# Kernel tuning notes

Hardware: AMD Instinct MI355X
Metric: run time of the kernel (lower is better)

Reference implementation:

```python
import jax, jax.numpy as jnp
import numpy as np

B, S, D = 2, 1024, 2048
H, KV, HD = 16, 4, 128
GROUPS = H // KV
THETA = 10000.0


def act_quant(xr, xi):
    # per-token 8-bit absmax quantization over last dim, joint scale for re/im, STE
    amax = jnp.maximum(jnp.max(jnp.abs(xr), -1, keepdims=True),
                       jnp.max(jnp.abs(xi), -1, keepdims=True))
    s = 127.0 / jnp.maximum(amax, 1e-5)
    qr = jnp.clip(jnp.round(xr * s), -128, 127) / s
    qi = jnp.clip(jnp.round(xi * s), -128, 127) / s
    return xr + jax.lax.stop_gradient(qr - xr), xi + jax.lax.stop_gradient(qi - xi)


def weight_quant(wr, wi):
    # Fairy+-i direction quantization: each weight -> scale * d, d in {+1,-1,+i,-i}; STE
    mag = jnp.mean(jnp.sqrt(wr * wr + wi * wi))
    use_re = jnp.abs(wr) >= jnp.abs(wi)
    qr = jnp.where(use_re, jnp.sign(wr) * mag, 0.0)
    qi = jnp.where(use_re, 0.0, jnp.sign(wi) * mag)
    return wr + jax.lax.stop_gradient(qr - wr), wi + jax.lax.stop_gradient(qi - wi)


def complex_linear(xr, xi, wr, wi):
    xr, xi = act_quant(xr, xi)
    wr, wi = weight_quant(wr, wi)
    o_re = xr @ wr - xi @ wi
    o_im = xr @ wi + xi @ wr
    return o_re, o_im


def rotate_half(x):
    h = x.shape[-1] // 2
    return jnp.concatenate([-x[..., h:], x[..., :h]], axis=-1)


def rope_tables():
    inv_freq = 1.0 / (THETA ** (jnp.arange(0, HD, 2, dtype=jnp.float32) / HD))
    pos = jnp.arange(S, dtype=jnp.float32)
    freqs = pos[:, None] * inv_freq[None, :]          # [S, HD/2]
    emb = jnp.concatenate([freqs, freqs], axis=-1)    # [S, HD]
    return jnp.cos(emb)[None, None], jnp.sin(emb)[None, None]  # [1,1,S,HD]


def _heads(x, n):
    # [B,S,n*HD] -> [B,n,S,HD]
    return x.reshape(B, S, n, HD).transpose(0, 2, 1, 3)


def _attn(hidden_real, hidden_imag, wq_re, wq_im, wk_re, wk_im,
          wv_re, wv_im, wo_re, wo_im):
    q_re, q_im = complex_linear(hidden_real, hidden_imag, wq_re, wq_im)
    k_re, k_im = complex_linear(hidden_real, hidden_imag, wk_re, wk_im)
    v_re, v_im = complex_linear(hidden_real, hidden_imag, wv_re, wv_im)

    q_re, q_im = _heads(q_re, H), _heads(q_im, H)      # [B,H,S,HD]
    k_re, k_im = _heads(k_re, KV), _heads(k_im, KV)    # [B,KV,S,HD]
    v_re, v_im = _heads(v_re, KV), _heads(v_im, KV)

    cos, sin = rope_tables()
    # RoPE applied only to real components of q and k
    q_re = q_re * cos + rotate_half(q_re) * sin
    k_re = k_re * cos + rotate_half(k_re) * sin

    # GQA repeat
    k_re = jnp.repeat(k_re, GROUPS, axis=1)
    k_im = jnp.repeat(k_im, GROUPS, axis=1)
    v_re = jnp.repeat(v_re, GROUPS, axis=1)
    v_im = jnp.repeat(v_im, GROUPS, axis=1)

    # real scores = Re(q . conj(k)) = q_re.k_re + q_im.k_im
    scores = (jnp.einsum('bhqd,bhkd->bhqk', q_re, k_re) +
              jnp.einsum('bhqd,bhkd->bhqk', q_im, k_im)) / jnp.sqrt(jnp.float32(HD))
    causal = jnp.tril(jnp.ones((S, S), dtype=bool))
    scores = jnp.where(causal[None, None], scores, jnp.finfo(scores.dtype).min)
    attn = jax.nn.softmax(scores, axis=-1)

    o_re = jnp.einsum('bhqk,bhkd->bhqd', attn, v_re)
    o_im = jnp.einsum('bhqk,bhkd->bhqd', attn, v_im)
    o_re = o_re.transpose(0, 2, 1, 3).reshape(B, S, H * HD)
    o_im = o_im.transpose(0, 2, 1, 3).reshape(B, S, H * HD)

    out_re, out_im = complex_linear(o_re, o_im, wo_re, wo_im)
    return jnp.stack([out_re, out_im])  # [2,B,S,D]


def setup_inputs() -> dict:
    key = jax.random.key(0)
    ks = jax.random.split(key, 12)
    w = lambda k, shp: jax.random.normal(k, shp, dtype=jnp.float32) * 0.02
    return {
        'hidden_real': jax.random.normal(ks[0], (B, S, D), dtype=jnp.float32),
        'hidden_imag': jax.random.normal(ks[1], (B, S, D), dtype=jnp.float32),
        'wq_re': w(ks[2], (D, H * HD)), 'wq_im': w(ks[3], (D, H * HD)),
        'wk_re': w(ks[4], (D, KV * HD)), 'wk_im': w(ks[5], (D, KV * HD)),
        'wv_re': w(ks[6], (D, KV * HD)), 'wv_im': w(ks[7], (D, KV * HD)),
        'wo_re': w(ks[8], (H * HD, D)), 'wo_im': w(ks[9], (H * HD, D)),
    }


def reference(hidden_real, hidden_imag, wq_re, wq_im, wk_re, wk_im,
              wv_re, wv_im, wo_re, wo_im):
    return _attn(hidden_real, hidden_imag, wq_re, wq_im, wk_re, wk_im,
                 wv_re, wv_im, wo_re, wo_im)
```

## Files before the change

kernel.cpp:

```cpp
#include <hip/hip_runtime.h>
#include <stdint.h>

#define B_   2
#define S_   1024
#define D_   2048
#define H_   16
#define KV_  4
#define HD_  128
#define NTOK (B_ * S_)
#define QD   (H_ * HD_)
#define KD   (KV_ * HD_)

using i32x4  = __attribute__((ext_vector_type(4)))  int;
using i32x16 = __attribute__((ext_vector_type(16))) int;
using f32x4  = __attribute__((ext_vector_type(4)))  float;
using bf16x8 = __attribute__((ext_vector_type(8)))  short;

#define LN1E4_OVER_64 0.14391156831212725f

__device__ __forceinline__ float bf2f(uint16_t u) { return __uint_as_float((uint32_t)u << 16); }
__device__ __forceinline__ uint16_t f2bf(float f) {
    uint32_t u = __float_as_uint(f);
    return (uint16_t)((u + 0x7FFFu + ((u >> 16) & 1u)) >> 16);
}

__global__ __launch_bounds__(256)
void act_quant_i8_kernel(const float* __restrict__ xr, const float* __restrict__ xi,
                         int8_t* __restrict__ qr, int8_t* __restrict__ qi,
                         float* __restrict__ invs)
{
    const int tok = blockIdx.x, t = threadIdx.x;
    const float* pr = xr + (size_t)tok * 2048 + t * 8;
    const float* pi = xi + (size_t)tok * 2048 + t * 8;
    float4 r0 = *(const float4*)pr, r1 = *(const float4*)(pr + 4);
    float4 i0 = *(const float4*)pi, i1 = *(const float4*)(pi + 4);
    float am = fmaxf(fmaxf(fmaxf(fabsf(r0.x), fabsf(r0.y)), fmaxf(fabsf(r0.z), fabsf(r0.w))),
                     fmaxf(fmaxf(fabsf(r1.x), fabsf(r1.y)), fmaxf(fabsf(r1.z), fabsf(r1.w))));
    am = fmaxf(am, fmaxf(fmaxf(fmaxf(fabsf(i0.x), fabsf(i0.y)), fmaxf(fabsf(i0.z), fabsf(i0.w))),
                         fmaxf(fmaxf(fabsf(i1.x), fabsf(i1.y)), fmaxf(fabsf(i1.z), fabsf(i1.w)))));
    __shared__ float red[256];
    red[t] = am;
    __syncthreads();
    for (int st = 128; st > 0; st >>= 1) {
        if (t < st) red[t] = fmaxf(red[t], red[t + st]);
        __syncthreads();
    }
    const float s = 127.0f / fmaxf(red[0], 1e-5f);
    if (t == 0) invs[tok] = 1.0f / s;
#define Q8(x) ((uint32_t)(uint8_t)(int8_t)(int)fminf(fmaxf(rintf((x) * s), -128.f), 127.f))
    uint32_t a0 = Q8(r0.x) | (Q8(r0.y) << 8) | (Q8(r0.z) << 16) | (Q8(r0.w) << 24);
    uint32_t a1 = Q8(r1.x) | (Q8(r1.y) << 8) | (Q8(r1.z) << 16) | (Q8(r1.w) << 24);
    uint32_t b0 = Q8(i0.x) | (Q8(i0.y) << 8) | (Q8(i0.z) << 16) | (Q8(i0.w) << 24);
    uint32_t b1 = Q8(i1.x) | (Q8(i1.y) << 8) | (Q8(i1.z) << 16) | (Q8(i1.w) << 24);
#undef Q8
    *(uint32_t*)(qr + (size_t)tok * 2048 + t * 8)     = a0;
    *(uint32_t*)(qr + (size_t)tok * 2048 + t * 8 + 4) = a1;
    *(uint32_t*)(qi + (size_t)tok * 2048 + t * 8)     = b0;
    *(uint32_t*)(qi + (size_t)tok * 2048 + t * 8 + 4) = b1;
}

__global__ __launch_bounds__(256)
void decode_kernel(const float* __restrict__ wr, const float* __restrict__ wi,
                   int N, int8_t* __restrict__ psr, int8_t* __restrict__ psi,
                   int8_t* __restrict__ pnsi, int n_off, float* __restrict__ mag_out)
{
    __shared__ alignas(16) int8_t tr[3][64][80];
    __shared__ float red[256];
    const int n0 = blockIdx.x * 64, k0 = blockIdx.y * 64;
    float msum = 0.f;
    for (int idx = threadIdx.x; idx < 4096; idx += 256) {
        int j = idx & 63, i = idx >> 6;
        size_t g = (size_t)(k0 + i) * N + n0 + j;
        float a = wr[g], b = wi[g];
        msum += sqrtf(a * a + b * b);
        int8_t sr, si;
        if (fabsf(a) >= fabsf(b)) {
            sr = (a > 0.f) ? 1 : ((a < 0.f) ? -1 : 0);
            si = 0;
        } else {
            sr = 0;
            si = (b > 0.f) ? 1 : ((b < 0.f) ? -1 : 0);
        }
        tr[0][j][i] = sr;
        tr[1][j][i] = si;
        tr[2][j][i] = (int8_t)(-si);
    }
    red[threadIdx.x] = msum;
    __syncthreads();
    for (int st = 128; st > 0; st >>= 1) {
        if (threadIdx.x < st) red[threadIdx.x] += red[threadIdx.x + st];
        __syncthreads();
    }
    if (threadIdx.x == 0) atomicAdd(mag_out, red[0]);
    int8_t* planes[3] = { psr, psi, pnsi };
    for (int idx = threadIdx.x; idx < 768; idx += 256) {
        int p = idx >> 8, rem = idx & 255, n = rem >> 2, c = rem & 3;
        int4 v = *(const int4*)&tr[p][n][c * 16];
        *(int4*)(planes[p] + (size_t)(n_off + n0 + n) * 2048 + k0 + c * 16) = v;
    }
}

__device__ __forceinline__ void async_copy16(const void* g, void* l) {
    __builtin_amdgcn_global_load_lds((const __attribute__((address_space(1))) void*)g,
                                     (__attribute__((address_space(3))) void*)l, 16, 0, 0);
}

template <int MODE>
__global__ __launch_bounds__(256)
void gemm_i8_kernel(const int8_t* __restrict__ axr, const int8_t* __restrict__ axi,
                    const int8_t* __restrict__ bsr, const int8_t* __restrict__ bsi,
                    const int8_t* __restrict__ bnsi,
                    int Nout, const float* __restrict__ invs,
                    const float* __restrict__ mag_sums,
                    float magc0, float magc1, float magc2,
                    float* o_re, float* o_im,
                    uint16_t* kbr, uint16_t* kbi, uint16_t* vbr, uint16_t* vbi)
{
    __shared__ alignas(16) int8_t smem[2][5 * 8192];
    const int tid = threadIdx.x;
    const int wav = tid >> 6, lane = tid & 63;
    const int tileM = blockIdx.y * 128, tileN = blockIdx.x * 128;
    const int wm = wav & 1, wn = wav >> 1;
    const int K = 2048;

    const int8_t* gplane[5] = { axr, axi, bsr, bsi, bnsi };
    const int     rbase[5]  = { tileM, tileM, tileN, tileN, tileN };

    i32x16 acc_re[2][2] = {};
    i32x16 acc_im[2][2] = {};

    auto issue_tile = [&](int k0, int buf) {
#pragma unroll
        for (int i = 0; i < 10; ++i) {
            int q = wav + 4 * i;
            int pl = q >> 3, seg = q & 7;
            int c = seg >> 1, m0 = (seg & 1) << 6;
            const int8_t* g = gplane[pl] + (size_t)(rbase[pl] + m0 + lane) * K + k0 + c * 16;
            int8_t* l = &smem[buf][pl * 8192 + (c * 128 + m0) * 16];
            async_copy16(g, l);
        }
    };

    issue_tile(0, 0);
    issue_tile(64, 1);

    for (int k = 0; k < 32; ++k) {
        if (k == 31) { asm volatile("s_waitcnt vmcnt(0)" ::: "memory"); }
        else         { asm volatile("s_waitcnt vmcnt(10)" ::: "memory"); }
        asm volatile("s_barrier" ::: "memory");
        const int8_t* sb = smem[k & 1];
#pragma unroll
        for (int s = 0; s < 2; ++s) {
            const int cc = 2 * s + (lane >> 5);
            const int rA = wm * 64 + (lane & 31);
            const int rB = wn * 64 + (lane & 31);
            i32x4 fxr[2], fxi[2], fsr[2], fsi[2], fns[2];
#pragma unroll
            for (int mb = 0; mb < 2; ++mb) {
                int off = (cc * 128 + rA + mb * 32) * 16;
                fxr[mb] = *(const i32x4*)&sb[0 * 8192 + off];
                fxi[mb] = *(const i32x4*)&sb[1 * 8192 + off];
            }
#pragma unroll
            for (int nb = 0; nb < 2; ++nb) {
                int off = (cc * 128 + rB + nb * 32) * 16;
                fsr[nb] = *(const i32x4*)&sb[2 * 8192 + off];
                fsi[nb] = *(const i32x4*)&sb[3 * 8192 + off];
                fns[nb] = *(const i32x4*)&sb[4 * 8192 + off];
            }
#pragma unroll
            for (int mb = 0; mb < 2; ++mb)
#pragma unroll
                for (int nb = 0; nb < 2; ++nb) {
                    acc_re[mb][nb] = __builtin_amdgcn_mfma_i32_32x32x32_i8(fxr[mb], fsr[nb], acc_re[mb][nb], 0, 0, 0);
                    acc_re[mb][nb] = __builtin_amdgcn_mfma_i32_32x32x32_i8(fxi[mb], fns[nb], acc_re[mb][nb], 0, 0, 0);
                    acc_im[mb][nb] = __builtin_amdgcn_mfma_i32_32x32x32_i8(fxr[mb], fsi[nb], acc_im[mb][nb], 0, 0, 0);
                    acc_im[mb][nb] = __builtin_amdgcn_mfma_i32_32x32x32_i8(fxi[mb], fsr[nb], acc_im[mb][nb], 0, 0, 0);
                }
        }
        asm volatile("s_barrier" ::: "memory");
        if (k + 2 < 32) issue_tile((k + 2) * 64, k & 1);
    }

    const int ln31 = lane & 31, lq = lane >> 5;
#pragma unroll
    for (int mb = 0; mb < 2; ++mb) {
#pragma unroll
        for (int nb = 0; nb < 2; ++nb) {
            const int gn = tileN + wn * 64 + nb * 32 + ln31;
            float mag;
            if (MODE == 0)
                mag = (gn < 2048) ? mag_sums[0] * magc0
                    : (gn < 2560) ? mag_sums[1] * magc1
                                  : mag_sums[2] * magc2;
            else
                mag = mag_sums[0] * magc0;
#pragma unroll
            for (int r = 0; r < 16; ++r) {
                const int row = (r & 3) + 8 * (r >> 2) + 4 * lq;
                const int gm = tileM + wm * 64 + mb * 32 + row;
                const float sc = mag * invs[gm];
                const float re = (float)acc_re[mb][nb][r] * sc;
                const float im = (float)acc_im[mb][nb][r] * sc;
                if (MODE == 1) {
                    o_re[(size_t)gm * Nout + gn] = re;
                    o_im[(size_t)gm * Nout + gn] = im;
                } else {
                    const int s = gm & (S_ - 1), bb = gm >> 10;
                    if (gn < 2048) {
                        o_re[(size_t)gm * 2048 + gn] = re;
                        o_im[(size_t)gm * 2048 + gn] = im;
                    } else if (gn < 2560) {
                        int c = gn - 2048, kvh = c >> 7, d = c & 127;
                        size_t off = ((size_t)(bb * KV_ + kvh) * S_ + s) * 128 + d;
                        kbr[off] = f2bf(re);
                        kbi[off] = f2bf(im);
                    } else {
                        int c = gn - 2560, kvh = c >> 7, d = c & 127;
                        size_t off = ((size_t)(bb * KV_ + kvh) * S_ + s) * 128 + d;
                        vbr[off] = f2bf(re);
                        vbi[off] = f2bf(im);
                    }
                }
            }
        }
    }
}

__global__ __launch_bounds__(256)
void rope_q_kernel(const float* __restrict__ q_re, const float* __restrict__ q_im,
                   uint16_t* __restrict__ qb_re, uint16_t* __restrict__ qb_im)
{
    int gidx = blockIdx.x * 256 + threadIdx.x;
    int j = gidx & 15, h = (gidx >> 4) & 15, tok = gidx >> 8;
    int s = tok & (S_ - 1), b = tok >> 10;
    int d0 = j * 4;
    size_t ib = (size_t)tok * 2048 + h * 128;
    float4 r0 = *(const float4*)&q_re[ib + d0];
    float4 r1 = *(const float4*)&q_re[ib + d0 + 64];
    float4 i0 = *(const float4*)&q_im[ib + d0];
    float4 i1 = *(const float4*)&q_im[ib + d0 + 64];
    float ro0[4], ro1[4];
    float rv0[4] = { r0.x, r0.y, r0.z, r0.w };
    float rv1[4] = { r1.x, r1.y, r1.z, r1.w };
#pragma unroll
    for (int t = 0; t < 4; ++t) {
        float f = __expf(-(float)(d0 + t) * LN1E4_OVER_64);
        float sn, c;
        __sincosf((float)s * f, &sn, &c);
        ro0[t] = rv0[t] * c - rv1[t] * sn;
        ro1[t] = rv1[t] * c + rv0[t] * sn;
    }
    size_t ob = ((size_t)(b * H_ + h) * S_ + s) * 128;
    ushort4 w;
    w = (ushort4){ f2bf(ro0[0]), f2bf(ro0[1]), f2bf(ro0[2]), f2bf(ro0[3]) };
    *(ushort4*)&qb_re[ob + d0] = w;
    w = (ushort4){ f2bf(ro1[0]), f2bf(ro1[1]), f2bf(ro1[2]), f2bf(ro1[3]) };
    *(ushort4*)&qb_re[ob + d0 + 64] = w;
    w = (ushort4){ f2bf(i0.x), f2bf(i0.y), f2bf(i0.z), f2bf(i0.w) };
    *(ushort4*)&qb_im[ob + d0] = w;
    w = (ushort4){ f2bf(i1.x), f2bf(i1.y), f2bf(i1.z), f2bf(i1.w) };
    *(ushort4*)&qb_im[ob + d0 + 64] = w;
}

__global__ __launch_bounds__(256)
void rope_k_kernel(uint16_t* __restrict__ kb_re)
{
    int gidx = blockIdx.x * 256 + threadIdx.x;
    int j = gidx & 15, kvh = (gidx >> 4) & 3;
    int rest = gidx >> 6;
    int s = rest & (S_ - 1), b = rest >> 10;
    int d0 = j * 4;
    size_t base = ((size_t)(b * KV_ + kvh) * S_ + s) * 128;
    ushort4 u0 = *(const ushort4*)&kb_re[base + d0];
    ushort4 u1 = *(const ushort4*)&kb_re[base + d0 + 64];
    float rv0[4] = { bf2f(u0.x), bf2f(u0.y), bf2f(u0.z), bf2f(u0.w) };
    float rv1[4] = { bf2f(u1.x), bf2f(u1.y), bf2f(u1.z), bf2f(u1.w) };
    float ro0[4], ro1[4];
#pragma unroll
    for (int t = 0; t < 4; ++t) {
        float f = __expf(-(float)(d0 + t) * LN1E4_OVER_64);
        float sn, c;
        __sincosf((float)s * f, &sn, &c);
        ro0[t] = rv0[t] * c - rv1[t] * sn;
        ro1[t] = rv1[t] * c + rv0[t] * sn;
    }
    *(ushort4*)&kb_re[base + d0]      = (ushort4){ f2bf(ro0[0]), f2bf(ro0[1]), f2bf(ro0[2]), f2bf(ro0[3]) };
    *(ushort4*)&kb_re[base + d0 + 64] = (ushort4){ f2bf(ro1[0]), f2bf(ro1[1]), f2bf(ro1[2]), f2bf(ro1[3]) };
}

__global__ __launch_bounds__(256)
void vtrans_kernel(const uint16_t* __restrict__ vbr, const uint16_t* __restrict__ vbi,
                   uint16_t* __restrict__ vtr, uint16_t* __restrict__ vti)
{
    __shared__ uint16_t t[32][36];
    const int pl = blockIdx.z & 1, bk = blockIdx.z >> 1;
    const int s0 = blockIdx.x * 32, d0 = blockIdx.y * 32;
    const uint16_t* src = (pl ? vbi : vbr) + ((size_t)bk * S_) * 128;
    uint16_t*       dst = (pl ? vti : vtr) + ((size_t)bk * 128) * S_;
    const int r = threadIdx.x >> 3, c = (threadIdx.x & 7) * 4;
    *(ushort4*)&t[r][c] = *(const ushort4*)&src[(size_t)(s0 + r) * 128 + d0 + c];
    __syncthreads();
    ushort4 o = (ushort4){ t[c][r], t[c + 1][r], t[c + 2][r], t[c + 3][r] };
    *(ushort4*)&dst[(size_t)(d0 + r) * S_ + s0 + c] = o;
}

__global__ __launch_bounds__(256)
void attn_mfma_kernel(const uint16_t* __restrict__ qb_re, const uint16_t* __restrict__ qb_im,
                      const uint16_t* __restrict__ kb_re, const uint16_t* __restrict__ kb_im,
                      const uint16_t* __restrict__ vt_re, const uint16_t* __restrict__ vt_im,
                      float* __restrict__ o_re, float* __restrict__ o_im)
{
    __shared__ alignas(16) uint16_t sbuf[2][16384];
    __shared__ alignas(16) uint16_t sp[4][16][40];

    const int tid = threadIdx.x;
    const int w = tid >> 6, lane = tid & 63;
    const int r16 = lane & 15, q4 = lane >> 4;
    const int qt = gridDim.x - 1 - blockIdx.x;
    const int h = blockIdx.y, b = blockIdx.z;
    const int kvh = h >> 2;
    const int q0 = qt * 64, qw0 = q0 + w * 16;

    bf16x8 qfr[4], qfi[4];
    {
        const size_t qbase = ((size_t)(b * H_ + h) * S_ + qw0 + r16) * 128;
#pragma unroll
        for (int ks = 0; ks < 4; ++ks) {
            const int col = ks * 32 + q4 * 8;
            qfr[ks] = *(const bf16x8*)&qb_re[qbase + col];
            qfi[ks] = *(const bf16x8*)&qb_im[qbase + col];
        }
    }

    f32x4 oa[2][8] = {};
    float m_r[4] = { -3e38f, -3e38f, -3e38f, -3e38f };
    float l_r[4] = { 0.f, 0.f, 0.f, 0.f };

    const size_t kgbase0 = (size_t)(b * KV_ + kvh) * S_ * 128;
    const uint16_t* vre = vt_re + (size_t)(b * KV_ + kvh) * 128 * (size_t)S_;
    const uint16_t* vim = vt_im + (size_t)(b * KV_ + kvh) * 128 * (size_t)S_;

    const uint16_t* kp[4];
    const uint16_t* vp[4];
#pragma unroll
    for (int i = 0; i < 4; ++i) {
        const int kch = (i & 1) * 8 + w * 2 + (lane >> 5);
        kp[i] = ((i >> 1) ? kb_im : kb_re) + kgbase0 + (size_t)(lane & 31) * 128 + kch * 8;
        const int vch = (i & 1) * 2 + (w >> 1);
        const int vd  = ((w & 1) << 6) | lane;
        vp[i] = ((i >> 1) ? vim : vre) + (size_t)vd * S_ + vch * 8;
    }

    auto issue_tile = [&](int kt, int buf) {
#pragma unroll
        for (int i = 0; i < 4; ++i)
            async_copy16(kp[i] + (size_t)kt * 4096, &sbuf[buf][w * 512 + i * 2048]);
#pragma unroll
        for (int i = 0; i < 4; ++i)
            async_copy16(vp[i] + (size_t)kt * 32, &sbuf[buf][8192 + w * 512 + i * 2048]);
    };

    const int nk = (q0 + 64) >> 5;

    issue_tile(0, 0);
    issue_tile(1, 1);

    for (int k = 0; k < nk; ++k) {
        if (k == nk - 1) { asm volatile("s_waitcnt vmcnt(0)" ::: "memory"); }
        else             { asm volatile("s_waitcnt vmcnt(8)" ::: "memory"); }
        asm volatile("s_barrier" ::: "memory");
        const uint16_t* sb = sbuf[k & 1];
        const int c0 = k << 5;

        if (c0 <= qw0 + 15) {
            f32x4 sc[2] = {};
#pragma unroll
            for (int cblk = 0; cblk < 2; ++cblk) {
                const int krow = cblk * 16 + r16;
#pragma unroll
                for (int ks = 0; ks < 4; ++ks) {
                    const int koff = (ks * 4 + q4) * 256 + krow * 8;
                    bf16x8 kr = *(const bf16x8*)&sb[koff];
                    bf16x8 ki = *(const bf16x8*)&sb[4096 + koff];
                    sc[cblk] = __builtin_amdgcn_mfma_f32_16x16x32_bf16(qfr[ks], kr, sc[cblk], 0, 0, 0);
                    sc[cblk] = __builtin_amdgcn_mfma_f32_16x16x32_bf16(qfi[ks], ki, sc[cblk], 0, 0, 0);
                }
            }
#pragma unroll
            for (int cblk = 0; cblk < 2; ++cblk)
#pragma unroll
                for (int reg = 0; reg < 4; ++reg) {
                    float sval = sc[cblk][reg] * 0.08838834764831845f;
                    const int rowg = qw0 + q4 * 4 + reg;
                    const int colg = c0 + cblk * 16 + r16;
                    if (colg > rowg) sval = -3e38f;
                    sc[cblk][reg] = sval;
                }
            float al[4];
#pragma unroll
            for (int reg = 0; reg < 4; ++reg) {
                float mx = fmaxf(sc[0][reg], sc[1][reg]);
#pragma unroll
                for (int msk = 1; msk < 16; msk <<= 1) mx = fmaxf(mx, __shfl_xor(mx, msk));
                const float mn = fmaxf(m_r[reg], mx);
                al[reg] = __expf(m_r[reg] - mn);
                const float p0 = __expf(sc[0][reg] - mn);
                const float p1 = __expf(sc[1][reg] - mn);
                sc[0][reg] = p0; sc[1][reg] = p1;
                float rs = p0 + p1;
#pragma unroll
                for (int msk = 1; msk < 16; msk <<= 1) rs += __shfl_xor(rs, msk);
                l_r[reg] = l_r[reg] * al[reg] + rs;
                m_r[reg] = mn;
            }
#pragma unroll
            for (int cblk = 0; cblk < 2; ++cblk)
#pragma unroll
                for (int reg = 0; reg < 4; ++reg)
                    sp[w][q4 * 4 + reg][cblk * 16 + r16] = f2bf(sc[cblk][reg]);
#pragma unroll
            for (int dblk = 0; dblk < 8; ++dblk)
#pragma unroll
                for (int reg = 0; reg < 4; ++reg) {
                    oa[0][dblk][reg] *= al[reg];
                    oa[1][dblk][reg] *= al[reg];
                }
            bf16x8 pf = *(const bf16x8*)&sp[w][r16][q4 * 8];
#pragma unroll
            for (int dblk = 0; dblk < 8; ++dblk) {
                const int voff = 8192 + q4 * 1024 + (dblk * 16 + r16) * 8;
                bf16x8 vr = *(const bf16x8*)&sb[voff];
                bf16x8 vi = *(const bf16x8*)&sb[4096 + voff];
                oa[0][dblk] = __builtin_amdgcn_mfma_f32_16x16x32_bf16(pf, vr, oa[0][dblk], 0, 0, 0);
                oa[1][dblk] = __builtin_amdgcn_mfma_f32_16x16x32_bf16(pf, vi, oa[1][dblk], 0, 0, 0);
            }
        }

        asm volatile("s_barrier" ::: "memory");
        if (k + 2 < nk) issue_tile(k + 2, k & 1);
    }

    float inv[4];
#pragma unroll
    for (int reg = 0; reg < 4; ++reg) inv[reg] = 1.f / l_r[reg];
#pragma unroll
    for (int dblk = 0; dblk < 8; ++dblk) {
        const int col = h * 128 + dblk * 16 + r16;
#pragma unroll
        for (int reg = 0; reg < 4; ++reg) {
            const size_t tok = (size_t)b * S_ + qw0 + q4 * 4 + reg;
            o_re[tok * 2048 + col] = oa[0][dblk][reg] * inv[reg];
            o_im[tok * 2048 + col] = oa[1][dblk][reg] * inv[reg];
        }
    }
}

extern "C" void kernel_launch(void* const* d_in, const int* in_sizes, int n_in,
                              void* d_out, int out_size, void* d_ws, size_t ws_size,
                              hipStream_t stream)
{
    const float* hr    = (const float*)d_in[0];
    const float* hi    = (const float*)d_in[1];
    const float* wq_re = (const float*)d_in[2];
    const float* wq_im = (const float*)d_in[3];
    const float* wk_re = (const float*)d_in[4];
    const float* wk_im = (const float*)d_in[5];
    const float* wv_re = (const float*)d_in[6];
    const float* wv_im = (const float*)d_in[7];
    const float* wo_re = (const float*)d_in[8];
    const float* wo_im = (const float*)d_in[9];
    float* out = (float*)d_out;
    char*  base = (char*)d_ws;

    const size_t MB4  = (size_t)2048 * 2048;
    const size_t QKVP = (size_t)3072 * 2048;
    const size_t KVE  = (size_t)B_ * KV_ * S_ * 128;

    float*   mags   = (float*)(base);
    float*   invs1  = (float*)(base + 1024);
    float*   invs2  = (float*)(base + 9216);
    int8_t*  xr_q   = (int8_t*)(base + 32768);
    int8_t*  xi_q   = xr_q + MB4;
    int8_t*  qkv_sr = xi_q + MB4;
    int8_t*  qkv_si = qkv_sr + QKVP;
    int8_t*  qkv_ns = qkv_si + QKVP;
    int8_t*  wo_sr  = qkv_ns + QKVP;
    int8_t*  wo_si  = wo_sr + MB4;
    int8_t*  wo_ns  = wo_si + MB4;
    float*   q_re   = (float*)(wo_ns + MB4);
    float*   q_im   = q_re + MB4;
    uint16_t* kb_re = (uint16_t*)(q_im + MB4);
    uint16_t* kb_im = kb_re + KVE;
    uint16_t* vb_re = kb_im + KVE;
    uint16_t* vb_im = vb_re + KVE;
    uint16_t* vt_re = (uint16_t*)xr_q;
    uint16_t* vt_im = (uint16_t*)xi_q;
    uint16_t* qb_re = (uint16_t*)qkv_sr;
    uint16_t* qb_im = (uint16_t*)(qkv_sr + 8388608);

    hipMemsetAsync(mags, 0, 16, stream);

    decode_kernel<<<dim3(32, 32), 256, 0, stream>>>(wq_re, wq_im, 2048, qkv_sr, qkv_si, qkv_ns, 0,    mags + 0);
    decode_kernel<<<dim3(8, 32),  256, 0, stream>>>(wk_re, wk_im, 512,  qkv_sr, qkv_si, qkv_ns, 2048, mags + 1);
    decode_kernel<<<dim3(8, 32),  256, 0, stream>>>(wv_re, wv_im, 512,  qkv_sr, qkv_si, qkv_ns, 2560, mags + 2);
    decode_kernel<<<dim3(32, 32), 256, 0, stream>>>(wo_re, wo_im, 2048, wo_sr, wo_si, wo_ns, 0,       mags + 3);

    act_quant_i8_kernel<<<NTOK, 256, 0, stream>>>(hr, hi, xr_q, xi_q, invs1);

    gemm_i8_kernel<0><<<dim3(24, 16), 256, 0, stream>>>(
        xr_q, xi_q, qkv_sr, qkv_si, qkv_ns, 0, invs1, mags,
        1.0f / (float)((size_t)D_ * QD), 1.0f / (float)((size_t)D_ * KD), 1.0f / (float)((size_t)D_ * KD),
        q_re, q_im, kb_re, kb_im, vb_re, vb_im);

    rope_q_kernel<<<NTOK * H_ * 16 / 256, 256, 0, stream>>>(q_re, q_im, qb_re, qb_im);
    rope_k_kernel<<<NTOK * KV_ * 16 / 256, 256, 0, stream>>>(kb_re);
    vtrans_kernel<<<dim3(S_ / 32, 128 / 32, B_ * KV_ * 2), 256, 0, stream>>>(vb_re, vb_im, vt_re, vt_im);

    attn_mfma_kernel<<<dim3(S_ / 64, H_, B_), 256, 0, stream>>>(
        qb_re, qb_im, kb_re, kb_im, vt_re, vt_im, q_re, q_im);

    act_quant_i8_kernel<<<NTOK, 256, 0, stream>>>(q_re, q_im, xr_q, xi_q, invs2);

    gemm_i8_kernel<1><<<dim3(16, 16), 256, 0, stream>>>(
        xr_q, xi_q, wo_sr, wo_si, wo_ns, 2048, invs2, mags + 3,
        1.0f / (float)((size_t)QD * D_), 0.f, 0.f,
        out, out + MB4, nullptr, nullptr, nullptr, nullptr);
}
```

Before: 495.1 us.

## Split int8 GEMM block across 8 waves with 64x32 per-wave tiles

The int8 complex GEMM now runs with 512 threads per block. Each of 8 waves computes a 64x32 sub-tile instead of a 64x64 one, and the async tile loads are redistributed across the waves. This halves accumulator registers per wave and doubles the number of resident waves, aiming for better latency hiding and MFMA utilization. In exchange, A fragments are read from LDS by more waves and each wave issues fewer MFMAs per LDS read.

```diff
diff --git a/kernel.cpp b/kernel.cpp
--- a/kernel.cpp
+++ b/kernel.cpp
@@ -106,7 +106,7 @@
 }
 
 template <int MODE>
-__global__ __launch_bounds__(256)
+__global__ __launch_bounds__(512, 4)
 void gemm_i8_kernel(const int8_t* __restrict__ axr, const int8_t* __restrict__ axi,
                     const int8_t* __restrict__ bsr, const int8_t* __restrict__ bsi,
                     const int8_t* __restrict__ bnsi,
@@ -126,13 +126,13 @@
     const int8_t* gplane[5] = { axr, axi, bsr, bsi, bnsi };
     const int     rbase[5]  = { tileM, tileM, tileN, tileN, tileN };
 
-    i32x16 acc_re[2][2] = {};
-    i32x16 acc_im[2][2] = {};
+    i32x16 acc_re[2] = {};
+    i32x16 acc_im[2] = {};
 
     auto issue_tile = [&](int k0, int buf) {
 #pragma unroll
-        for (int i = 0; i < 10; ++i) {
-            int q = wav + 4 * i;
+        for (int i = 0; i < 5; ++i) {
+            int q = wav + 8 * i;
             int pl = q >> 3, seg = q & 7;
             int c = seg >> 1, m0 = (seg & 1) << 6;
             const int8_t* g = gplane[pl] + (size_t)(rbase[pl] + m0 + lane) * K + k0 + c * 16;
@@ -146,81 +146,75 @@
 
     for (int k = 0; k < 32; ++k) {
         if (k == 31) { asm volatile("s_waitcnt vmcnt(0)" ::: "memory"); }
-        else         { asm volatile("s_waitcnt vmcnt(10)" ::: "memory"); }
+        else         { asm volatile("s_waitcnt vmcnt(5)" ::: "memory"); }
         asm volatile("s_barrier" ::: "memory");
         const int8_t* sb = smem[k & 1];
 #pragma unroll
         for (int s = 0; s < 2; ++s) {
             const int cc = 2 * s + (lane >> 5);
             const int rA = wm * 64 + (lane & 31);
-            const int rB = wn * 64 + (lane & 31);
-            i32x4 fxr[2], fxi[2], fsr[2], fsi[2], fns[2];
+            const int rB = wn * 32 + (lane & 31);
+            i32x4 fxr[2], fxi[2], fsr, fsi, fns;
 #pragma unroll
             for (int mb = 0; mb < 2; ++mb) {
                 int off = (cc * 128 + rA + mb * 32) * 16;
                 fxr[mb] = *(const i32x4*)&sb[0 * 8192 + off];
                 fxi[mb] = *(const i32x4*)&sb[1 * 8192 + off];
             }
-#pragma unroll
-            for (int nb = 0; nb < 2; ++nb) {
-                int off = (cc * 128 + rB + nb * 32) * 16;
-                fsr[nb] = *(const i32x4*)&sb[2 * 8192 + off];
-                fsi[nb] = *(const i32x4*)&sb[3 * 8192 + off];
-                fns[nb] = *(const i32x4*)&sb[4 * 8192 + off];
-            }
-#pragma unroll
-            for (int mb = 0; mb < 2; ++mb)
-#pragma unroll
-                for (int nb = 0; nb < 2; ++nb) {
-                    acc_re[mb][nb] = __builtin_amdgcn_mfma_i32_32x32x32_i8(fxr[mb], fsr[nb], acc_re[mb][nb], 0, 0, 0);
-                    acc_re[mb][nb] = __builtin_amdgcn_mfma_i32_32x32x32_i8(fxi[mb], fns[nb], acc_re[mb][nb], 0, 0, 0);
-                    acc_im[mb][nb] = __builtin_amdgcn_mfma_i32_32x32x32_i8(fxr[mb], fsi[nb], acc_im[mb][nb], 0, 0, 0);
-                    acc_im[mb][nb] = __builtin_amdgcn_mfma_i32_32x32x32_i8(fxi[mb], fsr[nb], acc_im[mb][nb], 0, 0, 0);
-                }
+            {
+                int off = (cc * 128 + rB) * 16;
+                fsr = *(const i32x4*)&sb[2 * 8192 + off];
+                fsi = *(const i32x4*)&sb[3 * 8192 + off];
+                fns = *(const i32x4*)&sb[4 * 8192 + off];
+            }
+#pragma unroll
+            for (int mb = 0; mb < 2; ++mb) {
+                acc_re[mb] = __builtin_amdgcn_mfma_i32_32x32x32_i8(fxr[mb], fsr, acc_re[mb], 0, 0, 0);
+                acc_re[mb] = __builtin_amdgcn_mfma_i32_32x32x32_i8(fxi[mb], fns, acc_re[mb], 0, 0, 0);
+                acc_im[mb] = __builtin_amdgcn_mfma_i32_32x32x32_i8(fxr[mb], fsi, acc_im[mb], 0, 0, 0);
+                acc_im[mb] = __builtin_amdgcn_mfma_i32_32x32x32_i8(fxi[mb], fsr, acc_im[mb], 0, 0, 0);
+            }
         }
         asm volatile("s_barrier" ::: "memory");
         if (k + 2 < 32) issue_tile((k + 2) * 64, k & 1);
     }
 
     const int ln31 = lane & 31, lq = lane >> 5;
+    const int gn = tileN + wn * 32 + ln31;
+    float mag;
+    if (MODE == 0)
+        mag = (gn < 2048) ? mag_sums[0] * magc0
+            : (gn < 2560) ? mag_sums[1] * magc1
+                          : mag_sums[2] * magc2;
+    else
+        mag = mag_sums[0] * magc0;
 #pragma unroll
     for (int mb = 0; mb < 2; ++mb) {
 #pragma unroll
-        for (int nb = 0; nb < 2; ++nb) {
-            const int gn = tileN + wn * 64 + nb * 32 + ln31;
-            float mag;
-            if (MODE == 0)
-                mag = (gn < 2048) ? mag_sums[0] * magc0
-                    : (gn < 2560) ? mag_sums[1] * magc1
-                                  : mag_sums[2] * magc2;
-            else
-                mag = mag_sums[0] * magc0;
-#pragma unroll
-            for (int r = 0; r < 16; ++r) {
-                const int row = (r & 3) + 8 * (r >> 2) + 4 * lq;
-                const int gm = tileM + wm * 64 + mb * 32 + row;
-                const float sc = mag * invs[gm];
-                const float re = (float)acc_re[mb][nb][r] * sc;
-                const float im = (float)acc_im[mb][nb][r] * sc;
-                if (MODE == 1) {
-                    o_re[(size_t)gm * Nout + gn] = re;
-                    o_im[(size_t)gm * Nout + gn] = im;
+        for (int r = 0; r < 16; ++r) {
+            const int row = (r & 3) + 8 * (r >> 2) + 4 * lq;
+            const int gm = tileM + wm * 64 + mb * 32 + row;
+            const float sc = mag * invs[gm];
+            const float re = (float)acc_re[mb][r] * sc;
+            const float im = (float)acc_im[mb][r] * sc;
+            if (MODE == 1) {
+                o_re[(size_t)gm * Nout + gn] = re;
+                o_im[(size_t)gm * Nout + gn] = im;
+            } else {
+                const int s = gm & (S_ - 1), bb = gm >> 10;
+                if (gn < 2048) {
+                    o_re[(size_t)gm * 2048 + gn] = re;
+                    o_im[(size_t)gm * 2048 + gn] = im;
+                } else if (gn < 2560) {
+                    int c = gn - 2048, kvh = c >> 7, d = c & 127;
+                    size_t off = ((size_t)(bb * KV_ + kvh) * S_ + s) * 128 + d;
+                    kbr[off] = f2bf(re);
+                    kbi[off] = f2bf(im);
                 } else {
-                    const int s = gm & (S_ - 1), bb = gm >> 10;
-                    if (gn < 2048) {
-                        o_re[(size_t)gm * 2048 + gn] = re;
-                        o_im[(size_t)gm * 2048 + gn] = im;
-                    } else if (gn < 2560) {
-                        int c = gn - 2048, kvh = c >> 7, d = c & 127;
-                        size_t off = ((size_t)(bb * KV_ + kvh) * S_ + s) * 128 + d;
-                        kbr[off] = f2bf(re);
-                        kbi[off] = f2bf(im);
-                    } else {
-                        int c = gn - 2560, kvh = c >> 7, d = c & 127;
-                        size_t off = ((size_t)(bb * KV_ + kvh) * S_ + s) * 128 + d;
-                        vbr[off] = f2bf(re);
-                        vbi[off] = f2bf(im);
-                    }
+                    int c = gn - 2560, kvh = c >> 7, d = c & 127;
+                    size_t off = ((size_t)(bb * KV_ + kvh) * S_ + s) * 128 + d;
+                    vbr[off] = f2bf(re);
+                    vbi[off] = f2bf(im);
                 }
             }
         }
@@ -508,7 +502,7 @@
 
     act_quant_i8_kernel<<<NTOK, 256, 0, stream>>>(hr, hi, xr_q, xi_q, invs1);
 
-    gemm_i8_kernel<0><<<dim3(24, 16), 256, 0, stream>>>(
+    gemm_i8_kernel<0><<<dim3(24, 16), 512, 0, stream>>>(
         xr_q, xi_q, qkv_sr, qkv_si, qkv_ns, 0, invs1, mags,
         1.0f / (float)((size_t)D_ * QD), 1.0f / (float)((size_t)D_ * KD), 1.0f / (float)((size_t)D_ * KD),
         q_re, q_im, kb_re, kb_im, vb_re, vb_im);
@@ -522,7 +516,7 @@
 
     act_quant_i8_kernel<<<NTOK, 256, 0, stream>>>(q_re, q_im, xr_q, xi_q, invs2);
 
-    gemm_i8_kernel<1><<<dim3(16, 16), 256, 0, stream>>>(
+    gemm_i8_kernel<1><<<dim3(16, 16), 512, 0, stream>>>(
         xr_q, xi_q, wo_sr, wo_si, wo_ns, 2048, invs2, mags + 3,
         1.0f / (float)((size_t)QD * D_), 0.f, 0.f,
         out, out + MB4, nullptr, nullptr, nullptr, nullptr);
```

New measurement: 486.5 us. Within noise of the previous version (-1.7%).
